# Optimization experiments

Hardware: AMD Instinct MI355X
Metric: run time of the kernel (lower is better)

The kernel has to match this reference:

```python
import jax, jax.numpy as jnp
import numpy as np

T = 127  # SEQ_LENGTH - 1
VOCAB = 512
HID = 1024
BATCH = 256


def leaky_scan(x, beta):
    """StateLeaky: v[t] = beta * v[t-1] + x[t], v[-1]=0. x: [T,B,H], beta: [H]."""
    def step(v, xt):
        v = beta * v + xt
        return v, v
    _, out = jax.lax.scan(step, jnp.zeros_like(x[0]), x)
    return out


def setup_inputs() -> dict:
    key = jax.random.key(0)
    ks = jax.random.split(key, 9)
    s1 = 1.0 / np.sqrt(VOCAB)
    s2 = 1.0 / np.sqrt(HID)
    x = jax.random.normal(ks[0], (T, BATCH, VOCAB), dtype=jnp.float32)
    W1 = jax.random.uniform(ks[1], (HID, VOCAB), jnp.float32, -s1, s1)
    b1 = jax.random.uniform(ks[2], (HID,), jnp.float32, -s1, s1)
    W2 = jax.random.uniform(ks[3], (HID, HID), jnp.float32, -s2, s2)
    b2 = jax.random.uniform(ks[4], (HID,), jnp.float32, -s2, s2)
    W3 = jax.random.uniform(ks[5], (HID, HID), jnp.float32, -s2, s2)
    b3 = jax.random.uniform(ks[6], (HID,), jnp.float32, -s2, s2)
    W4 = jax.random.uniform(ks[7], (VOCAB, HID), jnp.float32, -s2, s2)
    b4 = jax.random.uniform(ks[8], (VOCAB,), jnp.float32, -s2, s2)
    beta1 = jnp.full((HID,), 0.9, dtype=jnp.float32)
    beta2 = jnp.full((HID,), 0.9, dtype=jnp.float32)
    beta3 = jnp.full((HID,), 0.9, dtype=jnp.float32)
    return {"x": x, "W1": W1, "b1": b1, "beta1": beta1, "W2": W2, "b2": b2,
            "beta2": beta2, "W3": W3, "b3": b3, "beta3": beta3, "W4": W4, "b4": b4}


def reference(x, W1, b1, beta1, W2, b2, beta2, W3, b3, beta3, W4, b4):
    # fc1: [T,B,V] @ [V,H] -> [T,B,H]
    h = jnp.einsum('tbv,hv->tbh', x, W1) + b1
    h = leaky_scan(h, beta1)
    h = jax.nn.relu(jnp.einsum('tbh,gh->tbg', h, W2) + b2)
    h = leaky_scan(h, beta2)
    h = jax.nn.relu(jnp.einsum('tbh,gh->tbg', h, W3) + b3)
    h = leaky_scan(h, beta3)
    out = jnp.einsum('tbh,vh->tbv', h, W4) + b4  # [T,B,V]
    return out
```

## Files before the change

kernel.cpp:

```cpp
#include <hip/hip_runtime.h>

#define T_STEPS 127
#define BATCH   256
#define VOCAB   512
#define HID     1024
#define MROWS   (T_STEPS * BATCH)
#define BHID    (BATCH * HID)
#define BVOC    (BATCH * VOCAB)

typedef __attribute__((ext_vector_type(4))) float f32x4;
typedef __attribute__((ext_vector_type(8))) short s16x8;
typedef unsigned short u16;

__device__ __forceinline__ u16 f2bf(float f) {
    union { float f; unsigned u; } c; c.f = f;
    unsigned u = c.u;
    u += 0x7FFFu + ((u >> 16) & 1u);
    return (u16)(u >> 16);
}
__device__ __forceinline__ float bf2f(u16 x) {
    union { float f; unsigned u; } c; c.u = ((unsigned)x) << 16;
    return c.f;
}

__global__ __launch_bounds__(256) void cvtscan_kernel(const float* __restrict__ x,
                                                      u16* __restrict__ out,
                                                      const float* __restrict__ beta) {
    const float b = beta[0];
    const int base = blockIdx.x * 256 + threadIdx.x;
    float v = 0.f;
    const float* ip = x + base;
    u16*         op = out + base;
#pragma unroll 4
    for (int t = 0; t < T_STEPS; ++t) {
        v = b * v + *ip;
        *op = f2bf(v);
        ip += BVOC; op += BVOC;
    }
}

#define W1Q (HID * VOCAB / 4)
#define W2Q (W1Q + HID * HID / 4)
#define W3Q (W2Q + HID * HID / 4)
#define W4Q (W3Q + VOCAB * HID / 4)
__global__ __launch_bounds__(256) void wcvt_kernel(const float* __restrict__ w1,
                                                   const float* __restrict__ w2,
                                                   const float* __restrict__ w3,
                                                   const float* __restrict__ w4,
                                                   u16* o1, u16* o2, u16* o3, u16* o4) {
    int i = blockIdx.x * 256 + threadIdx.x;
    const float* s; u16* d; int off;
    if      (i < W1Q) { s = w1; d = o1; off = i; }
    else if (i < W2Q) { s = w2; d = o2; off = i - W1Q; }
    else if (i < W3Q) { s = w3; d = o3; off = i - W2Q; }
    else if (i < W4Q) { s = w4; d = o4; off = i - W3Q; }
    else return;
    f32x4 v = ((const f32x4*)s)[off];
    ushort4 o;
    o.x = f2bf(v[0]); o.y = f2bf(v[1]); o.z = f2bf(v[2]); o.w = f2bf(v[3]);
    ((ushort4*)d)[off] = o;
}

__global__ __launch_bounds__(256) void scan2_kernel(const u16* __restrict__ in,
                                                    u16* __restrict__ out,
                                                    const float* __restrict__ beta) {
    int i2   = blockIdx.x * 256 + threadIdx.x;
    int base = i2 * 2;
    int hh   = base & (HID - 1);
    float b0 = beta[hh], b1 = beta[hh + 1];
    float v0 = 0.f, v1 = 0.f;
    const u16* ip = in + base;
    u16*       op = out + base;
    for (int t = 0; t < T_STEPS; ++t) {
        ushort2 xv = *(const ushort2*)ip;
        v0 = b0 * v0 + bf2f(xv.x);
        v1 = b1 * v1 + bf2f(xv.y);
        ushort2 o; o.x = f2bf(v0); o.y = f2bf(v1);
        *(ushort2*)op = o;
        ip += BHID; op += BHID;
    }
}


#define GLDS16(g, l) __builtin_amdgcn_global_load_lds(                      \
        (const __attribute__((address_space(1))) void*)(g),                 \
        (__attribute__((address_space(3))) void*)(l), 16, 0, 0)

template <int RA, int RB, int QM, int QN, int VM, class S>
__device__ __forceinline__ void do_phase(const u16* lds, f32x4 (&acc)[8][4],
                                         s16x8 (&af)[2][4][2], s16x8 (&bf)[2][2][2],
                                         int ab, int bb, int sw0, int sw1,
                                         S&& stage) {
    if constexpr (RA >= 0) {
#pragma unroll
        for (int i = 0; i < 4; ++i) {
            const u16* p = lds + ab + (RA * 64 + i * 16) * 64;
            af[RA][i][0] = *(const s16x8*)(p + sw0);
            af[RA][i][1] = *(const s16x8*)(p + sw1);
        }
    }
    if constexpr (RB >= 0) {
#pragma unroll
        for (int j = 0; j < 2; ++j) {
            const u16* p = lds + bb + (RB * 32 + j * 16) * 64;
            bf[RB][j][0] = *(const s16x8*)(p + sw0);
            bf[RB][j][1] = *(const s16x8*)(p + sw1);
        }
    }
    stage();
    __builtin_amdgcn_sched_barrier(0);
    __builtin_amdgcn_s_barrier();
    asm volatile("s_waitcnt lgkmcnt(0)" ::: "memory");
    __builtin_amdgcn_sched_barrier(0);
    __builtin_amdgcn_s_setprio(1);
#pragma unroll
    for (int i = 0; i < 4; ++i)
#pragma unroll
        for (int j = 0; j < 2; ++j) {
            acc[QM * 4 + i][QN * 2 + j] = __builtin_amdgcn_mfma_f32_16x16x32_bf16(
                af[QM][i][0], bf[QN][j][0], acc[QM * 4 + i][QN * 2 + j], 0, 0, 0);
            acc[QM * 4 + i][QN * 2 + j] = __builtin_amdgcn_mfma_f32_16x16x32_bf16(
                af[QM][i][1], bf[QN][j][1], acc[QM * 4 + i][QN * 2 + j], 0, 0, 0);
        }
    __builtin_amdgcn_s_setprio(0);
    if constexpr (VM == 6) asm volatile("s_waitcnt vmcnt(6)" ::: "memory");
    if constexpr (VM == 4) asm volatile("s_waitcnt vmcnt(4)" ::: "memory");
    __builtin_amdgcn_s_barrier();
    __builtin_amdgcn_sched_barrier(0);
}

template <bool RELU, bool BSC, typename OutT>
__global__ __launch_bounds__(512, 2) void gemm8(const u16* __restrict__ A,
                                                const u16* __restrict__ B,
                                                const float* __restrict__ bias,
                                                OutT* __restrict__ C,
                                                int N, int K,
                                                const float* __restrict__ bsbeta) {
    __shared__ u16 lds[65536];

    const int tid  = threadIdx.x;
    const int wv   = tid >> 6;
    const int lane = tid & 63;
    const int wr   = wv >> 2;
    const int wc   = wv & 3;
    const int lr   = lane & 15;

    int nwg = gridDim.x, orig = blockIdx.x;
    int qq = nwg >> 3, rr = nwg & 7, xcd = orig & 7, lin = orig >> 3;
    int wg = (xcd < rr ? xcd * (qq + 1) : rr * (qq + 1) + (xcd - rr) * qq) + lin;

    const int NT = N >> 8;
    const int mt = wg / NT, nt = wg % NT;

    const u16* Ag = A + (size_t)mt * 256 * K;
    const u16* Bg = B + (size_t)nt * 256 * K;

    const int grow  = tid >> 3;
    const int gcol  = 8 * ((tid & 7) ^ (grow & 7));
    const int wbase = wv * 512;

#define STAGE_A(j, buf, kt) GLDS16(Ag + (size_t)((j) * 64 + grow) * K + (kt) + gcol, \
                                   lds + (buf) * 32768 + (j) * 4096 + wbase)
#define STAGE_B(j, buf, kt) GLDS16(Bg + (size_t)((j) * 64 + grow) * K + (kt) + gcol, \
                                   lds + (buf) * 32768 + 16384 + (j) * 4096 + wbase)

    const int sw0 = 8 * (((lane >> 4)) ^ (lane & 7));
    const int sw1 = 8 * ((4 | (lane >> 4)) ^ (lane & 7));
    const int arow = (wr * 128 + lr) * 64;
    const int brow = (wc * 64 + lr) * 64;

    f32x4 acc[8][4] = {};
    s16x8 af[2][4][2], bf[2][2][2];
    const int NKT = K >> 6;

    STAGE_A(0, 0, 0); STAGE_A(2, 0, 0);
    STAGE_B(0, 0, 0); STAGE_B(1, 0, 0); STAGE_B(2, 0, 0); STAGE_B(3, 0, 0);
    STAGE_A(1, 0, 0); STAGE_A(3, 0, 0);
    STAGE_A(0, 1, 64); STAGE_A(2, 1, 64);
    asm volatile("s_waitcnt vmcnt(4)" ::: "memory");
    __builtin_amdgcn_s_barrier();
    __builtin_amdgcn_sched_barrier(0);

    for (int t = 0; t < NKT; ++t) {
        const int buf = t & 1, nbuf = buf ^ 1;
        const int t1 = (t + 1 < NKT) ? t + 1 : NKT - 1;
        const int t2 = (t + 2 < NKT) ? t + 2 : NKT - 1;
        const int kt1 = t1 << 6, kt2 = t2 << 6;
        const int ab = buf * 32768 + arow;
        const int bb = buf * 32768 + 16384 + brow;

        do_phase<0, 0, 0, 0, 6>(lds, acc, af, bf, ab, bb, sw0, sw1, [&] {
            STAGE_B(0, nbuf, kt1); STAGE_B(1, nbuf, kt1);
            STAGE_B(2, nbuf, kt1); STAGE_B(3, nbuf, kt1);
        });
        do_phase<1, -1, 1, 0, -1>(lds, acc, af, bf, ab, bb, sw0, sw1, [&] {
            STAGE_A(1, nbuf, kt1); STAGE_A(3, nbuf, kt1);
        });
        do_phase<-1, 1, 0, 1, -1>(lds, acc, af, bf, ab, bb, sw0, sw1, [&] {
            STAGE_A(0, buf, kt2); STAGE_A(2, buf, kt2);
        });
        do_phase<-1, -1, 1, 1, 4>(lds, acc, af, bf, ab, bb, sw0, sw1, [&] {});
    }

    float bs = 1.f;
    if constexpr (BSC) {
        float b = bsbeta[0];
        bs = (1.f - __powf(b, (float)(mt + 1))) / (1.f - b);
    }
    const int r0 = mt * 256 + wr * 128 + ((lane >> 4) << 2);
    const int c0 = nt * 256 + wc * 64 + lr;
    float bb4[4];
#pragma unroll
    for (int n = 0; n < 4; ++n) bb4[n] = bias[c0 + n * 16] * bs;
#pragma unroll
    for (int m = 0; m < 8; ++m)
#pragma unroll
        for (int j = 0; j < 4; ++j) {
            size_t rowoff = (size_t)(r0 + m * 16 + j) * N + c0;
#pragma unroll
            for (int n = 0; n < 4; ++n) {
                float v = acc[m][n][j] + bb4[n];
                if (RELU) v = v > 0.f ? v : 0.f;
                if constexpr (sizeof(OutT) == 2) C[rowoff + n * 16] = (OutT)f2bf(v);
                else                             C[rowoff + n * 16] = v;
            }
        }
#undef STAGE_A
#undef STAGE_B
}

extern "C" void kernel_launch(void* const* d_in, const int* in_sizes, int n_in,
                              void* d_out, int out_size, void* d_ws, size_t ws_size,
                              hipStream_t stream) {
    const float* x   = (const float*)d_in[0];
    const float* W1  = (const float*)d_in[1];
    const float* b1  = (const float*)d_in[2];
    const float* bt1 = (const float*)d_in[3];
    const float* W2  = (const float*)d_in[4];
    const float* b2  = (const float*)d_in[5];
    const float* bt2 = (const float*)d_in[6];
    const float* W3  = (const float*)d_in[7];
    const float* b3  = (const float*)d_in[8];
    const float* bt3 = (const float*)d_in[9];
    const float* W4  = (const float*)d_in[10];
    const float* b4  = (const float*)d_in[11];

    char* ws = (char*)d_ws;
    u16* h  = (u16*)ws;
    u16* a2 = (u16*)(ws + (size_t)MROWS * HID * 2);
    u16* xs = (u16*)(ws + (size_t)MROWS * HID * 4);
    char* wp = ws + (size_t)MROWS * HID * 4 + (size_t)MROWS * VOCAB * 2;
    u16* W1b = (u16*)wp; wp += (size_t)HID * VOCAB * 2;
    u16* W2b = (u16*)wp; wp += (size_t)HID * HID * 2;
    u16* W3b = (u16*)wp; wp += (size_t)HID * HID * 2;
    u16* W4b = (u16*)wp;

    cvtscan_kernel<<<dim3(BVOC / 256), dim3(256), 0, stream>>>(x, xs, bt1);
    wcvt_kernel<<<dim3(W4Q / 256), dim3(256), 0, stream>>>(
        W1, W2, W3, W4, W1b, W2b, W3b, W4b);

    const int MT = MROWS / 256;

    gemm8<false, true, u16><<<dim3(MT * (HID / 256)), dim3(512), 0, stream>>>(
        xs, W1b, b1, h, HID, VOCAB, bt1);
    gemm8<true, false, u16><<<dim3(MT * (HID / 256)), dim3(512), 0, stream>>>(
        h, W2b, b2, a2, HID, HID, nullptr);
    scan2_kernel<<<dim3(BHID / 2 / 256), dim3(256), 0, stream>>>(a2, h, bt2);
    gemm8<true, false, u16><<<dim3(MT * (HID / 256)), dim3(512), 0, stream>>>(
        h, W3b, b3, a2, HID, HID, nullptr);
    scan2_kernel<<<dim3(BHID / 2 / 256), dim3(256), 0, stream>>>(a2, h, bt3);
    gemm8<false, false, float><<<dim3(MT * (VOCAB / 256)), dim3(512), 0, stream>>>(
        h, W4b, b4, (float*)d_out, VOCAB, HID, nullptr);
}
```

Baseline: 326.1 us.

## Switch to batch-major padded layout and fuse leaky scans into GEMM epilogue

Activations are reordered from time-major to batch-major with time padded to 128. Each 256-row GEMM tile then holds two full batch sequences, so the leaky scan can run inside the GEMM epilogue. The epilogue transposes the tile through LDS and each lane scans one column over time. This removes both standalone scan kernels and their round trips of activation traffic through global memory. The cost is a serial 127-step epilogue per lane, strided global stores, one padded timestep of extra GEMM work, and a transposing store in the final GEMM.

```diff
diff --git a/kernel.cpp b/kernel.cpp
--- a/kernel.cpp
+++ b/kernel.cpp
@@ -4,12 +4,13 @@
 #define BATCH   256
 #define VOCAB   512
 #define HID     1024
-#define MROWS   (T_STEPS * BATCH)
-#define BHID    (BATCH * HID)
+#define TPAD    128
+#define MPAD    (BATCH * TPAD)
 #define BVOC    (BATCH * VOCAB)
 
 typedef __attribute__((ext_vector_type(4))) float f32x4;
 typedef __attribute__((ext_vector_type(8))) short s16x8;
+typedef __attribute__((ext_vector_type(8))) unsigned short u16x8;
 typedef unsigned short u16;
 
 __device__ __forceinline__ u16 f2bf(float f) {
@@ -24,19 +25,21 @@
 }
 
 __global__ __launch_bounds__(256) void cvtscan_kernel(const float* __restrict__ x,
-                                                      u16* __restrict__ out,
+                                                      u16* __restrict__ xs,
                                                       const float* __restrict__ beta) {
     const float b = beta[0];
-    const int base = blockIdx.x * 256 + threadIdx.x;
+    const int idx = blockIdx.x * 256 + threadIdx.x;
+    const int v_  = idx & (VOCAB - 1);
+    const int bb  = idx >> 9;
+    const float* ip = x + idx;
+    u16* op = xs + (size_t)bb * TPAD * VOCAB + v_;
     float v = 0.f;
-    const float* ip = x + base;
-    u16*         op = out + base;
-#pragma unroll 4
     for (int t = 0; t < T_STEPS; ++t) {
         v = b * v + *ip;
         *op = f2bf(v);
-        ip += BVOC; op += BVOC;
-    }
+        ip += BVOC; op += VOCAB;
+    }
+    *op = 0;
 }
 
 #define W1Q (HID * VOCAB / 4)
@@ -61,26 +64,6 @@
     ((ushort4*)d)[off] = o;
 }
 
-__global__ __launch_bounds__(256) void scan2_kernel(const u16* __restrict__ in,
-                                                    u16* __restrict__ out,
-                                                    const float* __restrict__ beta) {
-    int i2   = blockIdx.x * 256 + threadIdx.x;
-    int base = i2 * 2;
-    int hh   = base & (HID - 1);
-    float b0 = beta[hh], b1 = beta[hh + 1];
-    float v0 = 0.f, v1 = 0.f;
-    const u16* ip = in + base;
-    u16*       op = out + base;
-    for (int t = 0; t < T_STEPS; ++t) {
-        ushort2 xv = *(const ushort2*)ip;
-        v0 = b0 * v0 + bf2f(xv.x);
-        v1 = b1 * v1 + bf2f(xv.y);
-        ushort2 o; o.x = f2bf(v0); o.y = f2bf(v1);
-        *(ushort2*)op = o;
-        ip += BHID; op += BHID;
-    }
-}
-
 
 #define GLDS16(g, l) __builtin_amdgcn_global_load_lds(                      \
         (const __attribute__((address_space(1))) void*)(g),                 \
@@ -129,13 +112,13 @@
     __builtin_amdgcn_sched_barrier(0);
 }
 
-template <bool RELU, bool BSC, typename OutT>
+template <bool RELU, bool BSC, bool SCAN, bool TOUT, typename OutT>
 __global__ __launch_bounds__(512, 2) void gemm8(const u16* __restrict__ A,
                                                 const u16* __restrict__ B,
                                                 const float* __restrict__ bias,
                                                 OutT* __restrict__ C,
                                                 int N, int K,
-                                                const float* __restrict__ bsbeta) {
+                                                const float* __restrict__ aux) {
     __shared__ u16 lds[65536];
 
     const int tid  = threadIdx.x;
@@ -144,6 +127,7 @@
     const int wr   = wv >> 2;
     const int wc   = wv & 3;
     const int lr   = lane & 15;
+    const int g    = lane >> 4;
 
     int nwg = gridDim.x, orig = blockIdx.x;
     int qq = nwg >> 3, rr = nwg & 7, xcd = orig & 7, lin = orig >> 3;
@@ -202,29 +186,88 @@
         do_phase<-1, -1, 1, 1, 4>(lds, acc, af, bf, ab, bb, sw0, sw1, [&] {});
     }
 
-    float bs = 1.f;
-    if constexpr (BSC) {
-        float b = bsbeta[0];
-        bs = (1.f - __powf(b, (float)(mt + 1))) / (1.f - b);
-    }
-    const int r0 = mt * 256 + wr * 128 + ((lane >> 4) << 2);
     const int c0 = nt * 256 + wc * 64 + lr;
     float bb4[4];
 #pragma unroll
-    for (int n = 0; n < 4; ++n) bb4[n] = bias[c0 + n * 16] * bs;
-#pragma unroll
-    for (int m = 0; m < 8; ++m)
-#pragma unroll
-        for (int j = 0; j < 4; ++j) {
-            size_t rowoff = (size_t)(r0 + m * 16 + j) * N + c0;
+    for (int n = 0; n < 4; ++n) bb4[n] = bias[c0 + n * 16];
+
+    if constexpr (SCAN) {
+        asm volatile("s_waitcnt vmcnt(0) lgkmcnt(0)" ::: "memory");
+        __builtin_amdgcn_s_barrier();
+        __builtin_amdgcn_sched_barrier(0);
+        char* reg = (char*)lds + wv * 16384;
+#pragma unroll
+        for (int m = 0; m < 8; ++m)
 #pragma unroll
             for (int n = 0; n < 4; ++n) {
-                float v = acc[m][n][j] + bb4[n];
-                if (RELU) v = v > 0.f ? v : 0.f;
-                if constexpr (sizeof(OutT) == 2) C[rowoff + n * 16] = (OutT)f2bf(v);
-                else                             C[rowoff + n * 16] = v;
+                const int col = n * 16 + lr;
+                float w0 = acc[m][n][0] + bb4[n];
+                float w1 = acc[m][n][1] + bb4[n];
+                float w2 = acc[m][n][2] + bb4[n];
+                float w3 = acc[m][n][3] + bb4[n];
+                if (RELU) {
+                    w0 = w0 > 0.f ? w0 : 0.f; w1 = w1 > 0.f ? w1 : 0.f;
+                    w2 = w2 > 0.f ? w2 : 0.f; w3 = w3 > 0.f ? w3 : 0.f;
+                }
+                uint2 pk;
+                pk.x = (unsigned)f2bf(w0) | ((unsigned)f2bf(w1) << 16);
+                pk.y = (unsigned)f2bf(w2) | ((unsigned)f2bf(w3) << 16);
+                const int toff = (m * 32 + g * 8) ^ ((col & 15) << 4);
+                *(uint2*)(reg + col * 256 + toff) = pk;
             }
+        asm volatile("s_waitcnt lgkmcnt(0)" ::: "memory");
+        __builtin_amdgcn_sched_barrier(0);
+        const int col = lane;
+        const float bs = aux[nt * 256 + wc * 64 + lane];
+        u16x8 rb[16];
+#pragma unroll
+        for (int k = 0; k < 16; ++k)
+            rb[k] = *(const u16x8*)(reg + col * 256 + ((k * 16) ^ ((col & 15) << 4)));
+        asm volatile("s_waitcnt lgkmcnt(0)" ::: "memory");
+        __builtin_amdgcn_sched_barrier(0);
+        float v = 0.f;
+        u16* gout = (u16*)C + (size_t)((2 * mt + wr) * TPAD) * N
+                  + nt * 256 + wc * 64 + lane;
+#pragma unroll
+        for (int t = 0; t < T_STEPS; ++t) {
+            v = bs * v + bf2f(rb[t >> 3][t & 7]);
+            gout[(size_t)t * N] = f2bf(v);
         }
+    } else if constexpr (TOUT) {
+        const int b_abs = 2 * mt + wr;
+#pragma unroll
+        for (int m = 0; m < 8; ++m)
+#pragma unroll
+            for (int j = 0; j < 4; ++j) {
+                const int t = m * 16 + g * 4 + j;
+                if (t < T_STEPS) {
+                    size_t ro = (size_t)t * (BATCH * VOCAB) + (size_t)b_abs * VOCAB + c0;
+#pragma unroll
+                    for (int n = 0; n < 4; ++n)
+                        ((float*)C)[ro + n * 16] = acc[m][n][j] + bb4[n];
+                }
+            }
+    } else {
+        const int r0 = mt * 256 + wr * 128 + g * 4;
+        float bbeta = BSC ? aux[0] : 0.f;
+#pragma unroll
+        for (int m = 0; m < 8; ++m)
+#pragma unroll
+            for (int j = 0; j < 4; ++j) {
+                float scl = 1.f;
+                if constexpr (BSC) {
+                    const int t = m * 16 + g * 4 + j;
+                    scl = (1.f - __powf(bbeta, (float)(t + 1))) / (1.f - bbeta);
+                }
+                size_t rowoff = (size_t)(r0 + m * 16 + j) * N + c0;
+#pragma unroll
+                for (int n = 0; n < 4; ++n) {
+                    float v = acc[m][n][j] + bb4[n] * scl;
+                    if (RELU) v = v > 0.f ? v : 0.f;
+                    ((u16*)C)[rowoff + n * 16] = f2bf(v);
+                }
+            }
+    }
 #undef STAGE_A
 #undef STAGE_B
 }
@@ -246,10 +289,10 @@
     const float* b4  = (const float*)d_in[11];
 
     char* ws = (char*)d_ws;
-    u16* h  = (u16*)ws;
-    u16* a2 = (u16*)(ws + (size_t)MROWS * HID * 2);
-    u16* xs = (u16*)(ws + (size_t)MROWS * HID * 4);
-    char* wp = ws + (size_t)MROWS * HID * 4 + (size_t)MROWS * VOCAB * 2;
+    u16* h1 = (u16*)ws;
+    u16* h2 = (u16*)(ws + (size_t)MPAD * HID * 2);
+    u16* xs = (u16*)(ws + (size_t)MPAD * HID * 4);
+    char* wp = ws + (size_t)MPAD * HID * 4 + (size_t)MPAD * VOCAB * 2;
     u16* W1b = (u16*)wp; wp += (size_t)HID * VOCAB * 2;
     u16* W2b = (u16*)wp; wp += (size_t)HID * HID * 2;
     u16* W3b = (u16*)wp; wp += (size_t)HID * HID * 2;
@@ -259,16 +302,18 @@
     wcvt_kernel<<<dim3(W4Q / 256), dim3(256), 0, stream>>>(
         W1, W2, W3, W4, W1b, W2b, W3b, W4b);
 
-    const int MT = MROWS / 256;
-
-    gemm8<false, true, u16><<<dim3(MT * (HID / 256)), dim3(512), 0, stream>>>(
-        xs, W1b, b1, h, HID, VOCAB, bt1);
-    gemm8<true, false, u16><<<dim3(MT * (HID / 256)), dim3(512), 0, stream>>>(
-        h, W2b, b2, a2, HID, HID, nullptr);
-    scan2_kernel<<<dim3(BHID / 2 / 256), dim3(256), 0, stream>>>(a2, h, bt2);
-    gemm8<true, false, u16><<<dim3(MT * (HID / 256)), dim3(512), 0, stream>>>(
-        h, W3b, b3, a2, HID, HID, nullptr);
-    scan2_kernel<<<dim3(BHID / 2 / 256), dim3(256), 0, stream>>>(a2, h, bt3);
-    gemm8<false, false, float><<<dim3(MT * (VOCAB / 256)), dim3(512), 0, stream>>>(
-        h, W4b, b4, (float*)d_out, VOCAB, HID, nullptr);
-}
+    const int MT = MPAD / 256;
+
+    gemm8<false, true, false, false, u16>
+        <<<dim3(MT * (HID / 256)), dim3(512), 0, stream>>>(
+        xs, W1b, b1, h1, HID, VOCAB, bt1);
+    gemm8<true, false, true, false, u16>
+        <<<dim3(MT * (HID / 256)), dim3(512), 0, stream>>>(
+        h1, W2b, b2, h2, HID, HID, bt2);
+    gemm8<true, false, true, false, u16>
+        <<<dim3(MT * (HID / 256)), dim3(512), 0, stream>>>(
+        h2, W3b, b3, h1, HID, HID, bt3);
+    gemm8<false, false, false, true, float>
+        <<<dim3(MT * (VOCAB / 256)), dim3(512), 0, stream>>>(
+        h1, W4b, b4, (float*)d_out, VOCAB, HID, nullptr);
+}
```

Result: faster. 299.7 us (-8.1%).
